# Kernel tuning notes

Hardware: AMD Instinct MI355X
Metric: run time of the kernel (lower is better)

Reference implementation:

```python
import jax, jax.numpy as jnp
import numpy as np

N_NODES = 25000
N_EDGES = 400000
N = 2          # per-node group dim (h.size(1))
IN_DIM = 64
HEADS = 4
HEAD_DIM = 16  # out_dim; HEADS*HEAD_DIM == IN_DIM here


def setup_inputs() -> dict:
    key = jax.random.key(0)
    ks = jax.random.split(key, 8)
    w_scale = 1.0 / np.sqrt(IN_DIM)
    return {
        "h": jax.random.normal(ks[0], (N_NODES, N, IN_DIM), jnp.float32),
        "e": jax.random.normal(ks[1], (N_EDGES, N, IN_DIM), jnp.float32),
        "W_Q": jax.random.normal(ks[2], (IN_DIM, HEADS * HEAD_DIM), jnp.float32) * w_scale,
        "W_K": jax.random.normal(ks[3], (IN_DIM, HEADS * HEAD_DIM), jnp.float32) * w_scale,
        "W_V": jax.random.normal(ks[4], (IN_DIM, HEADS * HEAD_DIM), jnp.float32) * w_scale,
        "W_repe": jax.random.normal(ks[5], (IN_DIM, HEADS * HEAD_DIM), jnp.float32) * w_scale,
        "src": jax.random.randint(ks[6], (N_EDGES,), 0, N_NODES, jnp.int32),
        "dst": jax.random.randint(ks[7], (N_EDGES,), 0, N_NODES, jnp.int32),
    }


def reference(h, e, W_Q, W_K, W_V, W_repe, src, dst):
    n_nodes, Nd, C = h.shape
    E = src.shape[0]
    # node-side projection Q_h: [n_nodes, N, H, D]
    Q_h = (h @ W_Q).reshape(n_nodes, Nd, HEADS, HEAD_DIM)
    # edge-side bias repe_e: [E, N, H, D]
    repe_e = (e @ W_repe).reshape(E, Nd, HEADS, HEAD_DIM)
    # compute_diff: relu(src - dst) on raw features  [E, N, C]
    diff = jax.nn.relu(h[src] - h[dst])
    k_diff = (diff @ W_K).reshape(E, Nd, HEADS, HEAD_DIM)
    v_diff = (diff @ W_V).reshape(E, Nd, HEADS, HEAD_DIM)
    # dst_cosim_diff: scale = ||k_diff|| * ||Q_h[dst]|| + 1e-6 (norm over last dim, keepdim)
    q_dst = Q_h[dst]  # [E, N, H, D]
    scale = (jnp.linalg.norm(k_diff, axis=-1, keepdims=True)
             * jnp.linalg.norm(q_dst, axis=-1, keepdims=True)) + 1e-6
    score = q_dst * k_diff * scale + repe_e
    msg = score * v_diff
    # update_all(copy_edge, max) -> segment max over dst; zero-degree nodes get 0 (DGL convention)
    h_out = jax.ops.segment_max(msg, dst, num_segments=n_nodes)
    h_out = jnp.where(jnp.isneginf(h_out), jnp.zeros((), h_out.dtype), h_out)
    return h_out
```

## Files before the change

### kernel.cpp

```cpp
#include <hip/hip_runtime.h>
#include <stdint.h>

#define N_NODES 25000
#define N_EDGES 400000

typedef __attribute__((ext_vector_type(8))) short short8;
typedef __attribute__((ext_vector_type(4))) float f32x4;

#define MFMA16(a, b, c) __builtin_amdgcn_mfma_f32_16x16x32_bf16((a), (b), (c), 0, 0, 0)

__device__ __forceinline__ short bf16r(float x) {
    unsigned u = __float_as_uint(x);
    u += 0x7FFFu + ((u >> 16) & 1u);
    return (short)(u >> 16);
}
__device__ __forceinline__ short bfr(float x) {
    return (short)((__float_as_uint(x) + 0x8000u) >> 16);
}

#define DPP_ADD(x, ctrl) \
    ((x) + __int_as_float(__builtin_amdgcn_update_dpp(0, __float_as_int(x), (ctrl), 0xF, 0xF, true)))
__device__ __forceinline__ float red16(float x) {
    x = DPP_ADD(x, 0xB1);
    x = DPP_ADD(x, 0x4E);
    x = DPP_ADD(x, 0x141);
    x = DPP_ADD(x, 0x140);
    return x;
}

__device__ __forceinline__ short8 load_bfrag(const float* __restrict__ W,
                                             int colbase, int lane, int khalf) {
    const int n = colbase + (lane & 15);
    const int k0 = khalf * 32 + ((lane >> 4) << 3);
    short8 f;
    #pragma unroll
    for (int j = 0; j < 8; ++j) f[j] = bf16r(W[(k0 + j) * 64 + n]);
    return f;
}

__device__ __forceinline__ short8 afrag(const short* S, int lane, int khalf) {
    return *(const short8*)&S[(lane & 15) * 72 + khalf * 32 + ((lane >> 4) << 3)];
}

__global__ __launch_bounds__(256) void zero_counts_kernel(int* __restrict__ counts) {
    const int i = blockIdx.x * 256 + threadIdx.x;
    if (i < N_NODES) counts[i] = 0;
}

__global__ __launch_bounds__(256) void hist_kernel(const int* __restrict__ dst,
                                                   int* __restrict__ counts) {
    const int i = blockIdx.x * 256 + threadIdx.x;
    if (i < N_EDGES) atomicAdd(&counts[dst[i]], 1);
}

#define BPT 98
__global__ __launch_bounds__(256) void scan_kernel(const int* __restrict__ counts,
                                                   int* __restrict__ offsets,
                                                   int* __restrict__ cursor) {
    __shared__ int part[256];
    const int t = threadIdx.x;
    const int base = t * BPT;
    int s = 0;
    for (int j = 0; j < BPT; ++j) {
        const int idx = base + j;
        if (idx < N_NODES) s += counts[idx];
    }
    part[t] = s;
    __syncthreads();
    for (int d = 1; d < 256; d <<= 1) {
        const int add = (t >= d) ? part[t - d] : 0;
        __syncthreads();
        part[t] += add;
        __syncthreads();
    }
    int run = (t > 0) ? part[t - 1] : 0;
    for (int j = 0; j < BPT; ++j) {
        const int idx = base + j;
        if (idx < N_NODES) {
            offsets[idx] = run;
            cursor[idx]  = run;
            run += counts[idx];
        }
    }
    if (t == 255) offsets[N_NODES] = part[255];
}

__global__ __launch_bounds__(256) void scatter_kernel(
    const int* __restrict__ src, const int* __restrict__ dst,
    int* __restrict__ cursor, int* __restrict__ perm, int* __restrict__ srcs) {
    const int i = blockIdx.x * 256 + threadIdx.x;
    if (i < N_EDGES) {
        const int d = dst[i];
        const int pos = atomicAdd(&cursor[d], 1);
        perm[pos] = i;
        srcs[pos] = src[i];
    }
}

__global__ __launch_bounds__(256) void q_mfma_kernel(
    const float* __restrict__ h, const float* __restrict__ Wq,
    const float* __restrict__ Wk, const float* __restrict__ Wv,
    const float* __restrict__ Wr, float* __restrict__ Q, short8* __restrict__ fw)
{
    __shared__ short sH[64 * 72];
    const int t = threadIdx.x;
    const int lane = t & 63, w = t >> 6;
    const int wcol = w << 4;
    const int ln = lane & 15, lq = lane >> 4;
    const int base = blockIdx.x * 64;

    const short8 b0 = load_bfrag(Wq, wcol, lane, 0);
    const short8 b1 = load_bfrag(Wq, wcol, lane, 1);

    {
        const int r = t >> 2, c4 = (t & 3) << 4;
        int row = base + r; if (row > 49999) row = 49999;
        const float4* p = (const float4*)&h[row * 64 + c4];
        short tmp[16];
        #pragma unroll
        for (int i = 0; i < 4; ++i) {
            float4 x = p[i];
            tmp[4*i+0] = bf16r(x.x); tmp[4*i+1] = bf16r(x.y);
            tmp[4*i+2] = bf16r(x.z); tmp[4*i+3] = bf16r(x.w);
        }
        *(short8*)&sH[r * 72 + c4]     = *(short8*)&tmp[0];
        *(short8*)&sH[r * 72 + c4 + 8] = *(short8*)&tmp[8];
    }
    __syncthreads();

    #pragma unroll
    for (int m = 0; m < 4; ++m) {
        const short* Sm = &sH[(m << 4) * 72];
        short8 a0 = afrag(Sm, lane, 0);
        short8 a1 = afrag(Sm, lane, 1);
        f32x4 acc = {0.f, 0.f, 0.f, 0.f};
        acc = MFMA16(a0, b0, acc);
        acc = MFMA16(a1, b1, acc);
        #pragma unroll
        for (int reg = 0; reg < 4; ++reg) {
            const int row = base + (m << 4) + (lq << 2) + reg;
            if (row < 50000) Q[row * 64 + wcol + ln] = acc[reg];
        }
    }

    if (blockIdx.x == 0) {
        fw[(w * 6 + 0) * 64 + lane] = load_bfrag(Wk, wcol, lane, 0);
        fw[(w * 6 + 1) * 64 + lane] = load_bfrag(Wk, wcol, lane, 1);
        fw[(w * 6 + 2) * 64 + lane] = load_bfrag(Wv, wcol, lane, 0);
        fw[(w * 6 + 3) * 64 + lane] = load_bfrag(Wv, wcol, lane, 1);
        fw[(w * 6 + 4) * 64 + lane] = load_bfrag(Wr, wcol, lane, 0);
        fw[(w * 6 + 5) * 64 + lane] = load_bfrag(Wr, wcol, lane, 1);
    }
}

__global__ __launch_bounds__(256, 2) void edge_wave_kernel(
    const float* __restrict__ h, const float* __restrict__ e,
    const float* __restrict__ Q, const int* __restrict__ srcs,
    const int* __restrict__ perm, const int* __restrict__ offsets,
    const short8* __restrict__ fw, float* __restrict__ out)
{
    __shared__ short sAll[4][2304];
    const int t = threadIdx.x;
    const int lane = t & 63, w = t >> 6;
    const int v = (blockIdx.x << 2) + w;
    short* SD = &sAll[w][0];
    short* SE = &sAll[w][1152];

    const int off0 = offsets[v];
    const int off1 = offsets[v + 1];
    const int deg  = off1 - off0;

    if (deg == 0) {
        out[(v << 7) + lane]      = 0.0f;
        out[(v << 7) + 64 + lane] = 0.0f;
        return;
    }

    const int ln = lane & 15, lq = lane >> 4;

    short8 bK0[4], bK1[4], bV0[4], bV1[4], bR0[4], bR1[4];
    #pragma unroll
    for (int hd = 0; hd < 4; ++hd) {
        bK0[hd] = fw[(hd * 6 + 0) * 64 + lane];
        bK1[hd] = fw[(hd * 6 + 1) * 64 + lane];
        bV0[hd] = fw[(hd * 6 + 2) * 64 + lane];
        bV1[hd] = fw[(hd * 6 + 3) * 64 + lane];
        bR0[hd] = fw[(hd * 6 + 4) * 64 + lane];
        bR1[hd] = fw[(hd * 6 + 5) * 64 + lane];
    }

    float q0[4], q1[4], qn0[4], qn1[4];
    #pragma unroll
    for (int hd = 0; hd < 4; ++hd) {
        q0[hd] = Q[(v << 7) + (hd << 4) + ln];
        q1[hd] = Q[(v << 7) + 64 + (hd << 4) + ln];
        qn0[hd] = sqrtf(red16(q0[hd] * q0[hd]));
        qn1[hd] = sqrtf(red16(q1[hd] * q1[hd]));
    }

    const int r = lane >> 2;
    const int cq = (lane & 3) << 4;
    const int n_r = r & 1;

    float4 xd[4];
    {
        const float4* pd = (const float4*)&h[(((v << 1) + n_r) << 6) + cq];
        xd[0] = pd[0]; xd[1] = pd[1]; xd[2] = pd[2]; xd[3] = pd[3];
    }

    const float NEG_INF = __uint_as_float(0xFF800000u);
    float rm0[4] = {NEG_INF, NEG_INF, NEG_INF, NEG_INF};
    float rm1[4] = {NEG_INF, NEG_INF, NEG_INF, NEG_INF};

    const int nch = (deg + 7) >> 3;
    for (int c = 0; c < nch; ++c) {
        int eidx = off0 + (c << 3) + (r >> 1);
        if (eidx > off1 - 1) eidx = off1 - 1;
        const int ed = perm[eidx];
        const int s  = srcs[eidx];
        const float4* ps = (const float4*)&h[(((s  << 1) + n_r) << 6) + cq];
        const float4* pe = (const float4*)&e[(((ed << 1) + n_r) << 6) + cq];

        short tmd[16], tme[16];
        #pragma unroll
        for (int i = 0; i < 4; ++i) {
            const float4 xs = ps[i], xe = pe[i];
            tmd[4*i+0] = bfr(fmaxf(xs.x - xd[i].x, 0.f));
            tmd[4*i+1] = bfr(fmaxf(xs.y - xd[i].y, 0.f));
            tmd[4*i+2] = bfr(fmaxf(xs.z - xd[i].z, 0.f));
            tmd[4*i+3] = bfr(fmaxf(xs.w - xd[i].w, 0.f));
            tme[4*i+0] = bfr(xe.x); tme[4*i+1] = bfr(xe.y);
            tme[4*i+2] = bfr(xe.z); tme[4*i+3] = bfr(xe.w);
        }
        *(short8*)&SD[r * 72 + cq]     = *(short8*)&tmd[0];
        *(short8*)&SD[r * 72 + cq + 8] = *(short8*)&tmd[8];
        *(short8*)&SE[r * 72 + cq]     = *(short8*)&tme[0];
        *(short8*)&SE[r * 72 + cq + 8] = *(short8*)&tme[8];

        __builtin_amdgcn_wave_barrier();

        const short8 a0 = afrag(SD, lane, 0);
        const short8 a1 = afrag(SD, lane, 1);
        const short8 g0 = afrag(SE, lane, 0);
        const short8 g1 = afrag(SE, lane, 1);

        #pragma unroll
        for (int hd = 0; hd < 4; ++hd) {
            f32x4 aK = {0.f, 0.f, 0.f, 0.f}, aV = aK, aR = aK;
            aK = MFMA16(a0, bK0[hd], aK); aK = MFMA16(a1, bK1[hd], aK);
            aV = MFMA16(a0, bV0[hd], aV); aV = MFMA16(a1, bV1[hd], aV);
            aR = MFMA16(g0, bR0[hd], aR); aR = MFMA16(g1, bR1[hd], aR);

            #pragma unroll
            for (int reg = 0; reg < 4; ++reg) {
                const int rl   = (lq << 2) + reg;
                const int eloc = rl >> 1;
                const int n2   = reg & 1;
                const bool valid = ((c << 3) + eloc) < deg;
                const float kk = aK[reg];
                const float sk = red16(kk * kk);
                const float scale = sqrtf(sk) * (n2 ? qn1[hd] : qn0[hd]) + 1e-6f;
                const float qv = n2 ? q1[hd] : q0[hd];
                float msg = (qv * kk * scale + aR[reg]) * aV[reg];
                msg = valid ? msg : NEG_INF;
                if (n2) rm1[hd] = fmaxf(rm1[hd], msg);
                else    rm0[hd] = fmaxf(rm0[hd], msg);
            }
        }
        __builtin_amdgcn_wave_barrier();
    }

    #pragma unroll
    for (int hd = 0; hd < 4; ++hd) {
        rm0[hd] = fmaxf(rm0[hd], __shfl_xor(rm0[hd], 16));
        rm0[hd] = fmaxf(rm0[hd], __shfl_xor(rm0[hd], 32));
        rm1[hd] = fmaxf(rm1[hd], __shfl_xor(rm1[hd], 16));
        rm1[hd] = fmaxf(rm1[hd], __shfl_xor(rm1[hd], 32));
    }
    const float o0 = (lq == 0) ? rm0[0] : (lq == 1) ? rm0[1] : (lq == 2) ? rm0[2] : rm0[3];
    const float o1 = (lq == 0) ? rm1[0] : (lq == 1) ? rm1[1] : (lq == 2) ? rm1[2] : rm1[3];
    out[(v << 7) + lane]      = o0;
    out[(v << 7) + 64 + lane] = o1;
}

extern "C" void kernel_launch(void* const* d_in, const int* in_sizes, int n_in,
                              void* d_out, int out_size, void* d_ws, size_t ws_size,
                              hipStream_t stream) {
    const float* h  = (const float*)d_in[0];
    const float* e  = (const float*)d_in[1];
    const float* Wq = (const float*)d_in[2];
    const float* Wk = (const float*)d_in[3];
    const float* Wv = (const float*)d_in[4];
    const float* Wr = (const float*)d_in[5];
    const int*   src = (const int*)d_in[6];
    const int*   dst = (const int*)d_in[7];
    float* out = (float*)d_out;

    float* Q       = (float*)d_ws;
    int*   counts  = (int*)d_ws + 3200000;
    int*   offsets = (int*)d_ws + 3225000;
    int*   cursor  = (int*)d_ws + 3250008;
    int*   perm    = (int*)d_ws + 3275008;
    int*   srcs    = (int*)d_ws + 3675008;
    short8* fw     = (short8*)((int*)d_ws + 4075008);

    zero_counts_kernel<<<98, 256, 0, stream>>>(counts);
    hist_kernel<<<1563, 256, 0, stream>>>(dst, counts);
    scan_kernel<<<1, 256, 0, stream>>>(counts, offsets, cursor);
    scatter_kernel<<<1563, 256, 0, stream>>>(src, dst, cursor, perm, srcs);
    q_mfma_kernel<<<782, 256, 0, stream>>>(h, Wq, Wk, Wv, Wr, Q, fw);
    edge_wave_kernel<<<6250, 256, 0, stream>>>(h, e, Q, srcs, perm, offsets, fw, out);
}
```

Baseline: 513.4 us.

## Fuse all stages into one persistent cooperative kernel with grid syncs

Replaces the six separate launches (zero, histogram, scan, scatter, Q projection, edge aggregation) with a single cooperative persistent kernel that uses grid.sync between phases. The single-block serial scan becomes a multi-block scan with per-block partial sums. The change targets launch overhead and the serialized one-block scan. In exchange it adds grid-wide barriers, and the edge phase loses the wide oversubscribed grid that helped hide its gather latency. If the cooperative launch fails, the code falls back to the old kernel sequence.

After: 634.0 us. 23.5% more time.

```diff
diff --git a/kernel.cpp b/kernel.cpp
--- a/kernel.cpp
+++ b/kernel.cpp
@@ -1,5 +1,8 @@
 #include <hip/hip_runtime.h>
+#include <hip/hip_cooperative_groups.h>
 #include <stdint.h>
+
+namespace cg = cooperative_groups;
 
 #define N_NODES 25000
 #define N_EDGES 400000
@@ -42,17 +45,250 @@
     return *(const short8*)&S[(lane & 15) * 72 + khalf * 32 + ((lane >> 4) << 3)];
 }
 
+__global__ __launch_bounds__(256, 2) void fused_kernel(
+    const float* __restrict__ h, const float* __restrict__ e,
+    const float* __restrict__ Wq, const float* __restrict__ Wk,
+    const float* __restrict__ Wv, const float* __restrict__ Wr,
+    const int* __restrict__ src, const int* __restrict__ dst,
+    float* __restrict__ Q, int* __restrict__ counts, int* __restrict__ offsets,
+    int* __restrict__ cursor, int* __restrict__ perm, int* __restrict__ srcs,
+    short8* __restrict__ fw, int* __restrict__ partials, float* __restrict__ out)
+{
+    cg::grid_group grid = cg::this_grid();
+    __shared__ __align__(16) char smem[18432];
+    const int t = threadIdx.x, b = blockIdx.x, G = gridDim.x;
+    const int lane = t & 63, w = t >> 6;
+    const int ln = lane & 15, lq = lane >> 4;
+
+    for (int i = b * 256 + t; i < N_NODES; i += G * 256) counts[i] = 0;
+    grid.sync();
+
+    for (int i = b * 256 + t; i < N_EDGES; i += G * 256) atomicAdd(&counts[dst[i]], 1);
+    {
+        short* sH = (short*)smem;
+        const int wcol = w << 4;
+        const short8 wb0 = load_bfrag(Wq, wcol, lane, 0);
+        const short8 wb1 = load_bfrag(Wq, wcol, lane, 1);
+        const int r = t >> 2, c4 = (t & 3) << 4;
+        for (int tile = b; tile < 782; tile += G) {
+            const int base = tile * 64;
+            __syncthreads();
+            {
+                int row = base + r; if (row > 49999) row = 49999;
+                const float4* p = (const float4*)&h[row * 64 + c4];
+                short tmp[16];
+                #pragma unroll
+                for (int i = 0; i < 4; ++i) {
+                    float4 x = p[i];
+                    tmp[4*i+0] = bf16r(x.x); tmp[4*i+1] = bf16r(x.y);
+                    tmp[4*i+2] = bf16r(x.z); tmp[4*i+3] = bf16r(x.w);
+                }
+                *(short8*)&sH[r * 72 + c4]     = *(short8*)&tmp[0];
+                *(short8*)&sH[r * 72 + c4 + 8] = *(short8*)&tmp[8];
+            }
+            __syncthreads();
+            #pragma unroll
+            for (int m = 0; m < 4; ++m) {
+                const short* Sm = &sH[(m << 4) * 72];
+                short8 a0 = afrag(Sm, lane, 0);
+                short8 a1 = afrag(Sm, lane, 1);
+                f32x4 acc = {0.f, 0.f, 0.f, 0.f};
+                acc = MFMA16(a0, wb0, acc);
+                acc = MFMA16(a1, wb1, acc);
+                #pragma unroll
+                for (int reg = 0; reg < 4; ++reg) {
+                    const int row = base + (m << 4) + (lq << 2) + reg;
+                    if (row < 50000) Q[row * 64 + wcol + ln] = acc[reg];
+                }
+            }
+        }
+        if (b == 0) {
+            fw[(w * 6 + 0) * 64 + lane] = load_bfrag(Wk, wcol, lane, 0);
+            fw[(w * 6 + 1) * 64 + lane] = load_bfrag(Wk, wcol, lane, 1);
+            fw[(w * 6 + 2) * 64 + lane] = load_bfrag(Wv, wcol, lane, 0);
+            fw[(w * 6 + 3) * 64 + lane] = load_bfrag(Wv, wcol, lane, 1);
+            fw[(w * 6 + 4) * 64 + lane] = load_bfrag(Wr, wcol, lane, 0);
+            fw[(w * 6 + 5) * 64 + lane] = load_bfrag(Wr, wcol, lane, 1);
+        }
+    }
+    grid.sync();
+
+    const int C = (N_NODES + G - 1) / G;
+    const int r0 = b * C;
+    int* sI = (int*)smem;
+    int cnt_t = 0;
+    if (t < C && (r0 + t) < N_NODES) cnt_t = counts[r0 + t];
+    __syncthreads();
+    sI[t] = cnt_t;
+    __syncthreads();
+    #pragma unroll
+    for (int d = 1; d < 256; d <<= 1) {
+        const int add = (t >= d) ? sI[t - d] : 0;
+        __syncthreads();
+        sI[t] += add;
+        __syncthreads();
+    }
+    const int incl  = sI[t];
+    const int total = sI[255];
+    if (t == 0) partials[b] = total;
+    grid.sync();
+
+    int pre = 0;
+    for (int j = t; j < b; j += 256) pre += partials[j];
+    __syncthreads();
+    sI[t] = pre;
+    __syncthreads();
+    #pragma unroll
+    for (int d = 128; d > 0; d >>= 1) {
+        if (t < d) sI[t] += sI[t + d];
+        __syncthreads();
+    }
+    pre = sI[0];
+    if (t < C && (r0 + t) < N_NODES) {
+        const int excl = pre + incl - cnt_t;
+        offsets[r0 + t] = excl;
+        cursor[r0 + t]  = excl;
+    }
+    if (b == 0 && t == 0) offsets[N_NODES] = N_EDGES;
+    grid.sync();
+
+    for (int i = b * 256 + t; i < N_EDGES; i += G * 256) {
+        const int d = dst[i];
+        const int pos = atomicAdd(&cursor[d], 1);
+        perm[pos] = i;
+        srcs[pos] = src[i];
+    }
+    grid.sync();
+
+    short* SD = (short*)smem + w * 2304;
+    short* SE = SD + 1152;
+
+    short8 bK0[4], bK1[4], bV0[4], bV1[4], bR0[4], bR1[4];
+    #pragma unroll
+    for (int hd = 0; hd < 4; ++hd) {
+        bK0[hd] = fw[(hd * 6 + 0) * 64 + lane];
+        bK1[hd] = fw[(hd * 6 + 1) * 64 + lane];
+        bV0[hd] = fw[(hd * 6 + 2) * 64 + lane];
+        bV1[hd] = fw[(hd * 6 + 3) * 64 + lane];
+        bR0[hd] = fw[(hd * 6 + 4) * 64 + lane];
+        bR1[hd] = fw[(hd * 6 + 5) * 64 + lane];
+    }
+
+    const int r  = lane >> 2;
+    const int cq = (lane & 3) << 4;
+    const int n_r = r & 1;
+    const float NEG_INF = __uint_as_float(0xFF800000u);
+
+    for (int v = (b << 2) + w; v < N_NODES; v += (G << 2)) {
+        const int off0 = offsets[v];
+        const int off1 = offsets[v + 1];
+        const int deg  = off1 - off0;
+
+        if (deg == 0) {
+            out[(v << 7) + lane]      = 0.0f;
+            out[(v << 7) + 64 + lane] = 0.0f;
+            continue;
+        }
+
+        float q0[4], q1[4], qn0[4], qn1[4];
+        #pragma unroll
+        for (int hd = 0; hd < 4; ++hd) {
+            q0[hd] = Q[(v << 7) + (hd << 4) + ln];
+            q1[hd] = Q[(v << 7) + 64 + (hd << 4) + ln];
+            qn0[hd] = sqrtf(red16(q0[hd] * q0[hd]));
+            qn1[hd] = sqrtf(red16(q1[hd] * q1[hd]));
+        }
+
+        float4 xd[4];
+        {
+            const float4* pd = (const float4*)&h[(((v << 1) + n_r) << 6) + cq];
+            xd[0] = pd[0]; xd[1] = pd[1]; xd[2] = pd[2]; xd[3] = pd[3];
+        }
+
+        float rm0[4] = {NEG_INF, NEG_INF, NEG_INF, NEG_INF};
+        float rm1[4] = {NEG_INF, NEG_INF, NEG_INF, NEG_INF};
+
+        const int nch = (deg + 7) >> 3;
+        for (int c = 0; c < nch; ++c) {
+            int eidx = off0 + (c << 3) + (r >> 1);
+            if (eidx > off1 - 1) eidx = off1 - 1;
+            const int ed = perm[eidx];
+            const int s  = srcs[eidx];
+            const float4* ps = (const float4*)&h[(((s  << 1) + n_r) << 6) + cq];
+            const float4* pe = (const float4*)&e[(((ed << 1) + n_r) << 6) + cq];
+
+            short tmd[16], tme[16];
+            #pragma unroll
+            for (int i = 0; i < 4; ++i) {
+                const float4 xs = ps[i], xe = pe[i];
+                tmd[4*i+0] = bfr(fmaxf(xs.x - xd[i].x, 0.f));
+                tmd[4*i+1] = bfr(fmaxf(xs.y - xd[i].y, 0.f));
+                tmd[4*i+2] = bfr(fmaxf(xs.z - xd[i].z, 0.f));
+                tmd[4*i+3] = bfr(fmaxf(xs.w - xd[i].w, 0.f));
+                tme[4*i+0] = bfr(xe.x); tme[4*i+1] = bfr(xe.y);
+                tme[4*i+2] = bfr(xe.z); tme[4*i+3] = bfr(xe.w);
+            }
+            *(short8*)&SD[r * 72 + cq]     = *(short8*)&tmd[0];
+            *(short8*)&SD[r * 72 + cq + 8] = *(short8*)&tmd[8];
+            *(short8*)&SE[r * 72 + cq]     = *(short8*)&tme[0];
+            *(short8*)&SE[r * 72 + cq + 8] = *(short8*)&tme[8];
+
+            __builtin_amdgcn_wave_barrier();
+
+            const short8 a0 = afrag(SD, lane, 0);
+            const short8 a1 = afrag(SD, lane, 1);
+            const short8 g0 = afrag(SE, lane, 0);
+            const short8 g1 = afrag(SE, lane, 1);
+
+            #pragma unroll
+            for (int hd = 0; hd < 4; ++hd) {
+                f32x4 aK = {0.f, 0.f, 0.f, 0.f}, aV = aK, aR = aK;
+                aK = MFMA16(a0, bK0[hd], aK); aK = MFMA16(a1, bK1[hd], aK);
+                aV = MFMA16(a0, bV0[hd], aV); aV = MFMA16(a1, bV1[hd], aV);
+                aR = MFMA16(g0, bR0[hd], aR); aR = MFMA16(g1, bR1[hd], aR);
+
+                #pragma unroll
+                for (int reg = 0; reg < 4; ++reg) {
+                    const int rl   = (lq << 2) + reg;
+                    const int eloc = rl >> 1;
+                    const int n2   = reg & 1;
+                    const bool valid = ((c << 3) + eloc) < deg;
+                    const float kk = aK[reg];
+                    const float sk = red16(kk * kk);
+                    const float scale = sqrtf(sk) * (n2 ? qn1[hd] : qn0[hd]) + 1e-6f;
+                    const float qv = n2 ? q1[hd] : q0[hd];
+                    float msg = (qv * kk * scale + aR[reg]) * aV[reg];
+                    msg = valid ? msg : NEG_INF;
+                    if (n2) rm1[hd] = fmaxf(rm1[hd], msg);
+                    else    rm0[hd] = fmaxf(rm0[hd], msg);
+                }
+            }
+            __builtin_amdgcn_wave_barrier();
+        }
+
+        #pragma unroll
+        for (int hd = 0; hd < 4; ++hd) {
+            rm0[hd] = fmaxf(rm0[hd], __shfl_xor(rm0[hd], 16));
+            rm0[hd] = fmaxf(rm0[hd], __shfl_xor(rm0[hd], 32));
+            rm1[hd] = fmaxf(rm1[hd], __shfl_xor(rm1[hd], 16));
+            rm1[hd] = fmaxf(rm1[hd], __shfl_xor(rm1[hd], 32));
+        }
+        const float o0 = (lq == 0) ? rm0[0] : (lq == 1) ? rm0[1] : (lq == 2) ? rm0[2] : rm0[3];
+        const float o1 = (lq == 0) ? rm1[0] : (lq == 1) ? rm1[1] : (lq == 2) ? rm1[2] : rm1[3];
+        out[(v << 7) + lane]      = o0;
+        out[(v << 7) + 64 + lane] = o1;
+    }
+}
+
 __global__ __launch_bounds__(256) void zero_counts_kernel(int* __restrict__ counts) {
     const int i = blockIdx.x * 256 + threadIdx.x;
     if (i < N_NODES) counts[i] = 0;
 }
-
 __global__ __launch_bounds__(256) void hist_kernel(const int* __restrict__ dst,
                                                    int* __restrict__ counts) {
     const int i = blockIdx.x * 256 + threadIdx.x;
     if (i < N_EDGES) atomicAdd(&counts[dst[i]], 1);
 }
-
 #define BPT 98
 __global__ __launch_bounds__(256) void scan_kernel(const int* __restrict__ counts,
                                                    int* __restrict__ offsets,
@@ -84,7 +320,6 @@
     }
     if (t == 255) offsets[N_NODES] = part[255];
 }
-
 __global__ __launch_bounds__(256) void scatter_kernel(
     const int* __restrict__ src, const int* __restrict__ dst,
     int* __restrict__ cursor, int* __restrict__ perm, int* __restrict__ srcs) {
@@ -96,7 +331,6 @@
         srcs[pos] = src[i];
     }
 }
-
 __global__ __launch_bounds__(256) void q_mfma_kernel(
     const float* __restrict__ h, const float* __restrict__ Wq,
     const float* __restrict__ Wk, const float* __restrict__ Wv,
@@ -108,10 +342,8 @@
     const int wcol = w << 4;
     const int ln = lane & 15, lq = lane >> 4;
     const int base = blockIdx.x * 64;
-
     const short8 b0 = load_bfrag(Wq, wcol, lane, 0);
     const short8 b1 = load_bfrag(Wq, wcol, lane, 1);
-
     {
         const int r = t >> 2, c4 = (t & 3) << 4;
         int row = base + r; if (row > 49999) row = 49999;
@@ -127,7 +359,6 @@
         *(short8*)&sH[r * 72 + c4 + 8] = *(short8*)&tmp[8];
     }
     __syncthreads();
-
     #pragma unroll
     for (int m = 0; m < 4; ++m) {
         const short* Sm = &sH[(m << 4) * 72];
@@ -142,7 +373,6 @@
             if (row < 50000) Q[row * 64 + wcol + ln] = acc[reg];
         }
     }
-
     if (blockIdx.x == 0) {
         fw[(w * 6 + 0) * 64 + lane] = load_bfrag(Wk, wcol, lane, 0);
         fw[(w * 6 + 1) * 64 + lane] = load_bfrag(Wk, wcol, lane, 1);
@@ -152,7 +382,6 @@
         fw[(w * 6 + 5) * 64 + lane] = load_bfrag(Wr, wcol, lane, 1);
     }
 }
-
 __global__ __launch_bounds__(256, 2) void edge_wave_kernel(
     const float* __restrict__ h, const float* __restrict__ e,
     const float* __restrict__ Q, const int* __restrict__ srcs,
@@ -165,19 +394,15 @@
     const int v = (blockIdx.x << 2) + w;
     short* SD = &sAll[w][0];
     short* SE = &sAll[w][1152];
-
     const int off0 = offsets[v];
     const int off1 = offsets[v + 1];
     const int deg  = off1 - off0;
-
     if (deg == 0) {
         out[(v << 7) + lane]      = 0.0f;
         out[(v << 7) + 64 + lane] = 0.0f;
         return;
     }
-
     const int ln = lane & 15, lq = lane >> 4;
-
     short8 bK0[4], bK1[4], bV0[4], bV1[4], bR0[4], bR1[4];
     #pragma unroll
     for (int hd = 0; hd < 4; ++hd) {
@@ -188,7 +413,6 @@
         bR0[hd] = fw[(hd * 6 + 4) * 64 + lane];
         bR1[hd] = fw[(hd * 6 + 5) * 64 + lane];
     }
-
     float q0[4], q1[4], qn0[4], qn1[4];
     #pragma unroll
     for (int hd = 0; hd < 4; ++hd) {
@@ -197,21 +421,17 @@
         qn0[hd] = sqrtf(red16(q0[hd] * q0[hd]));
         qn1[hd] = sqrtf(red16(q1[hd] * q1[hd]));
     }
-
     const int r = lane >> 2;
     const int cq = (lane & 3) << 4;
     const int n_r = r & 1;
-
     float4 xd[4];
     {
         const float4* pd = (const float4*)&h[(((v << 1) + n_r) << 6) + cq];
         xd[0] = pd[0]; xd[1] = pd[1]; xd[2] = pd[2]; xd[3] = pd[3];
     }
-
     const float NEG_INF = __uint_as_float(0xFF800000u);
     float rm0[4] = {NEG_INF, NEG_INF, NEG_INF, NEG_INF};
     float rm1[4] = {NEG_INF, NEG_INF, NEG_INF, NEG_INF};
-
     const int nch = (deg + 7) >> 3;
     for (int c = 0; c < nch; ++c) {
         int eidx = off0 + (c << 3) + (r >> 1);
@@ -220,7 +440,6 @@
         const int s  = srcs[eidx];
         const float4* ps = (const float4*)&h[(((s  << 1) + n_r) << 6) + cq];
         const float4* pe = (const float4*)&e[(((ed << 1) + n_r) << 6) + cq];
-
         short tmd[16], tme[16];
         #pragma unroll
         for (int i = 0; i < 4; ++i) {
@@ -236,21 +455,17 @@
         *(short8*)&SD[r * 72 + cq + 8] = *(short8*)&tmd[8];
         *(short8*)&SE[r * 72 + cq]     = *(short8*)&tme[0];
         *(short8*)&SE[r * 72 + cq + 8] = *(short8*)&tme[8];
-
         __builtin_amdgcn_wave_barrier();
-
         const short8 a0 = afrag(SD, lane, 0);
         const short8 a1 = afrag(SD, lane, 1);
         const short8 g0 = afrag(SE, lane, 0);
         const short8 g1 = afrag(SE, lane, 1);
-
         #pragma unroll
         for (int hd = 0; hd < 4; ++hd) {
             f32x4 aK = {0.f, 0.f, 0.f, 0.f}, aV = aK, aR = aK;
             aK = MFMA16(a0, bK0[hd], aK); aK = MFMA16(a1, bK1[hd], aK);
             aV = MFMA16(a0, bV0[hd], aV); aV = MFMA16(a1, bV1[hd], aV);
             aR = MFMA16(g0, bR0[hd], aR); aR = MFMA16(g1, bR1[hd], aR);
-
             #pragma unroll
             for (int reg = 0; reg < 4; ++reg) {
                 const int rl   = (lq << 2) + reg;
@@ -269,7 +484,6 @@
         }
         __builtin_amdgcn_wave_barrier();
     }
-
     #pragma unroll
     for (int hd = 0; hd < 4; ++hd) {
         rm0[hd] = fmaxf(rm0[hd], __shfl_xor(rm0[hd], 16));
@@ -296,18 +510,38 @@
     const int*   dst = (const int*)d_in[7];
     float* out = (float*)d_out;
 
-    float* Q       = (float*)d_ws;
-    int*   counts  = (int*)d_ws + 3200000;
-    int*   offsets = (int*)d_ws + 3225000;
-    int*   cursor  = (int*)d_ws + 3250008;
-    int*   perm    = (int*)d_ws + 3275008;
-    int*   srcs    = (int*)d_ws + 3675008;
-    short8* fw     = (short8*)((int*)d_ws + 4075008);
-
-    zero_counts_kernel<<<98, 256, 0, stream>>>(counts);
-    hist_kernel<<<1563, 256, 0, stream>>>(dst, counts);
-    scan_kernel<<<1, 256, 0, stream>>>(counts, offsets, cursor);
-    scatter_kernel<<<1563, 256, 0, stream>>>(src, dst, cursor, perm, srcs);
-    q_mfma_kernel<<<782, 256, 0, stream>>>(h, Wq, Wk, Wv, Wr, Q, fw);
-    edge_wave_kernel<<<6250, 256, 0, stream>>>(h, e, Q, srcs, perm, offsets, fw, out);
-}
+    float*  Q        = (float*)d_ws;
+    int*    counts   = (int*)d_ws + 3200000;
+    int*    offsets  = (int*)d_ws + 3225000;
+    int*    cursor   = (int*)d_ws + 3250008;
+    int*    perm     = (int*)d_ws + 3275008;
+    int*    srcs     = (int*)d_ws + 3675008;
+    short8* fw       = (short8*)((int*)d_ws + 4075008);
+    int*    partials = (int*)d_ws + 4081152;
+
+    int maxB = 0;
+    hipError_t qerr = hipOccupancyMaxActiveBlocksPerMultiprocessor(
+        &maxB, reinterpret_cast<const void*>(fused_kernel), 256, 0);
+    int G = (qerr == hipSuccess && maxB > 0) ? maxB * 256 : 0;
+    if (G > 2048) G = 2048;
+
+    hipError_t err = hipErrorUnknown;
+    if (G >= 98) {
+        void* args[] = {
+            (void*)&h, (void*)&e, (void*)&Wq, (void*)&Wk, (void*)&Wv, (void*)&Wr,
+            (void*)&src, (void*)&dst, (void*)&Q, (void*)&counts, (void*)&offsets,
+            (void*)&cursor, (void*)&perm, (void*)&srcs, (void*)&fw,
+            (void*)&partials, (void*)&out
+        };
+        err = hipLaunchCooperativeKernel(reinterpret_cast<const void*>(fused_kernel),
+                                         dim3(G), dim3(256), args, 0, stream);
+    }
+    if (err != hipSuccess) {
+        zero_counts_kernel<<<98, 256, 0, stream>>>(counts);
+        hist_kernel<<<1563, 256, 0, stream>>>(dst, counts);
+        scan_kernel<<<1, 256, 0, stream>>>(counts, offsets, cursor);
+        scatter_kernel<<<1563, 256, 0, stream>>>(src, dst, cursor, perm, srcs);
+        q_mfma_kernel<<<782, 256, 0, stream>>>(h, Wq, Wk, Wv, Wr, Q, fw);
+        edge_wave_kernel<<<6250, 256, 0, stream>>>(h, e, Q, srcs, perm, offsets, fw, out);
+    }
+}
```
